# Performance work log

Hardware: AMD Instinct MI355X
Metric: run time of the kernel (lower is better)

The kernel has to match this reference:

```python
import jax, jax.numpy as jnp
import numpy as np

NUM_HEADS = 16


def setup_inputs() -> dict:
    key = jax.random.key(0)
    ks = jax.random.split(key, 5)
    B, S, D = 2, 2048, 1024
    x = jax.random.normal(ks[0], (B, S, D), dtype=jnp.float32)
    # torch Linear weights are [out_features, in_features]; y = x @ W.T + b
    Wq = jax.random.normal(ks[1], (D, D), dtype=jnp.float32) * (D ** -0.5)
    Wk = jax.random.normal(ks[2], (D, D), dtype=jnp.float32) * (D ** -0.5)
    Wv = jax.random.normal(ks[3], (D, D), dtype=jnp.float32) * (D ** -0.5)
    Wo = jax.random.normal(ks[4], (D, D), dtype=jnp.float32) * (D ** -0.5)
    bo = jnp.zeros((D,), dtype=jnp.float32)
    return {"x": x, "Wq": Wq, "Wk": Wk, "Wv": Wv, "Wo": Wo, "bo": bo}


def reference(x, Wq, Wk, Wv, Wo, bo):
    B, S, D = x.shape
    H = NUM_HEADS
    dh = D // H
    # projections (torch Linear: x @ W.T)
    q = (x @ Wq.T).reshape(B, S, H, dh).transpose(0, 2, 1, 3)  # [B,H,S,dh]
    k = (x @ Wk.T).reshape(B, S, H, dh).transpose(0, 2, 1, 3)
    v = (x @ Wv.T).reshape(B, S, H, dh).transpose(0, 2, 1, 3)
    # NOTE: original code takes shape[-1] of the TRANSPOSED key (n,H,dh,S),
    # so the softmax scale is seq_length**-0.5 (a bug we reproduce faithfully).
    scale = jnp.asarray(S, x.dtype) ** -0.5
    scores = jnp.einsum("bhqd,bhkd->bhqk", q, k)  # [B,H,S,S]
    causal = jnp.triu(jnp.ones((S, S), dtype=bool), k=1)
    scores = jnp.where(causal, -jnp.inf, scores * scale)
    weights = jax.nn.softmax(scores, axis=-1)
    # dropout p=0.0 -> identity
    ctx = jnp.einsum("bhqk,bhkd->bhqd", weights, v)  # [B,H,S,dh]
    ctx = ctx.transpose(0, 2, 1, 3).reshape(B, S, D)
    return ctx @ Wo.T + bo
```

## Files before the change

kernel.cpp:

```cpp
#include <hip/hip_runtime.h>
#include <hip/hip_bf16.h>

#define B_SZ    2
#define S_LEN   2048
#define D_MODEL 1024
#define H_NUM   16
#define DH      64
#define M_TOT   (B_SZ * S_LEN)

#define QSCALE (0.022097086912079608f * 1.4426950408889634f)

typedef __attribute__((ext_vector_type(8)))  short          bf16x8;
typedef __attribute__((ext_vector_type(4)))  float          f32x4;
typedef __attribute__((ext_vector_type(16))) float          f32x16;
typedef __attribute__((ext_vector_type(8)))  unsigned short u16x8;
typedef __attribute__((ext_vector_type(4)))  unsigned short u16x4;

__device__ inline unsigned short f2bf(float f) {
  unsigned int u = __float_as_uint(f);
  u += 0x7fffu + ((u >> 16) & 1u);
  return (unsigned short)(u >> 16);
}

__device__ inline float bf2f(unsigned short u) {
  return __uint_as_float(((unsigned)u) << 16);
}

__device__ inline float fexp2(float x) {
#if __has_builtin(__builtin_amdgcn_exp2f)
  return __builtin_amdgcn_exp2f(x);
#else
  return exp2f(x);
#endif
}

__device__ inline unsigned cvt_pk_bf16(float lo, float hi) {
  unsigned r;
  asm("v_cvt_pk_bf16_f32 %0, %1, %2" : "=v"(r) : "v"(lo), "v"(hi));
  return r;
}

__device__ inline void gload16(const void* g, void* l) {
  __builtin_amdgcn_global_load_lds(
      (const __attribute__((address_space(1))) void*)g,
      (__attribute__((address_space(3))) void*)l, 16, 0, 0);
}

__global__ __launch_bounds__(256) void to_bf16_all(
    const float* __restrict__ x, const float* __restrict__ wq,
    const float* __restrict__ wk, const float* __restrict__ wv,
    const float* __restrict__ wo, unsigned short* __restrict__ xb,
    unsigned short* __restrict__ wqb, unsigned short* __restrict__ wkb,
    unsigned short* __restrict__ wvb, unsigned short* __restrict__ wob) {
  const size_t i = ((size_t)blockIdx.x * 256 + threadIdx.x) * 8;
  const float* src;
  unsigned short* dst;
  size_t off;
  if (i < 4194304)      { src = x;  dst = xb;  off = i; }
  else if (i < 5242880) { src = wq; dst = wqb; off = i - 4194304; }
  else if (i < 6291456) { src = wk; dst = wkb; off = i - 5242880; }
  else if (i < 7340032) { src = wv; dst = wvb; off = i - 6291456; }
  else                  { src = wo; dst = wob; off = i - 7340032; }
  f32x4 a = *(const f32x4*)(src + off);
  f32x4 b = *(const f32x4*)(src + off + 4);
  u16x8 o;
#pragma unroll
  for (int j = 0; j < 4; j++) { o[j] = f2bf(a[j]); o[4 + j] = f2bf(b[j]); }
  *(u16x8*)(dst + off) = o;
}

__device__ __forceinline__ void gemm_core(const unsigned short* __restrict__ A,
                                          const unsigned short* __restrict__ W,
                                          unsigned short (*Al)[128][32],
                                          unsigned short (*Bl)[128][32],
                                          int mbase, int nbase,
                                          f32x4 acc[4][4]) {
  const int tid  = threadIdx.x;
  const int lane = tid & 63;
  const int wid  = tid >> 6;
  const int wr   = wid >> 1, wc = wid & 1;
  const int g    = lane >> 4, lr = lane & 15;

  const int r0 = tid >> 2;
  const int cg = (tid & 3) ^ ((tid >> 3) & 3);

  const unsigned short* Abase = A + (size_t)(mbase + r0) * D_MODEL + cg * 8;
  const unsigned short* Wbase = W + (size_t)(nbase + r0) * D_MODEL + cg * 8;
  char* ldsA0 = (char*)Al + wid * 1024;
  char* ldsB0 = (char*)Bl + wid * 1024;

  gload16(Abase, ldsA0);
  gload16(Abase + (size_t)64 * D_MODEL, ldsA0 + 4096);
  gload16(Wbase, ldsB0);
  gload16(Wbase + (size_t)64 * D_MODEL, ldsB0 + 4096);
  gload16(Abase + 32, ldsA0 + 8192);
  gload16(Abase + (size_t)64 * D_MODEL + 32, ldsA0 + 8192 + 4096);
  gload16(Wbase + 32, ldsB0 + 8192);
  gload16(Wbase + (size_t)64 * D_MODEL + 32, ldsB0 + 8192 + 4096);

  const int NKT = D_MODEL / 32;
  int cur = 0, nx2 = 2;
  for (int kt = 0; kt < NKT; ++kt) {
    if (kt + 2 < NKT) {
      const unsigned short* As = Abase + (kt + 2) * 32;
      const unsigned short* Ws = Wbase + (kt + 2) * 32;
      char* la = ldsA0 + nx2 * 8192;
      char* lb = ldsB0 + nx2 * 8192;
      gload16(As, la);
      gload16(As + (size_t)64 * D_MODEL, la + 4096);
      gload16(Ws, lb);
      gload16(Ws + (size_t)64 * D_MODEL, lb + 4096);
      asm volatile("s_waitcnt vmcnt(8)" ::: "memory");
    } else if (kt + 1 < NKT) {
      asm volatile("s_waitcnt vmcnt(4)" ::: "memory");
    } else {
      asm volatile("s_waitcnt vmcnt(0)" ::: "memory");
    }
    __builtin_amdgcn_s_barrier();

    bf16x8 af[4], bfr[4];
#pragma unroll
    for (int i = 0; i < 4; i++) {
      const int ra = wr * 64 + i * 16 + lr;
      af[i] = *(const bf16x8*)&Al[cur][ra][(g ^ ((ra >> 1) & 3)) * 8];
      const int rb = wc * 64 + i * 16 + lr;
      bfr[i] = *(const bf16x8*)&Bl[cur][rb][(g ^ ((rb >> 1) & 3)) * 8];
    }
    __builtin_amdgcn_s_setprio(1);
#pragma unroll
    for (int i = 0; i < 4; i++)
#pragma unroll
      for (int j = 0; j < 4; j++)
        acc[i][j] = __builtin_amdgcn_mfma_f32_16x16x32_bf16(af[i], bfr[j],
                                                            acc[i][j], 0, 0, 0);
    __builtin_amdgcn_s_setprio(0);
    asm volatile("" ::: "memory");
    __builtin_amdgcn_s_barrier();
    cur = (cur == 2) ? 0 : cur + 1;
    nx2 = (nx2 == 2) ? 0 : nx2 + 1;
  }
}

__global__ __launch_bounds__(256) void gemm_qkv(
    const unsigned short* __restrict__ xb, const unsigned short* __restrict__ wqb,
    const unsigned short* __restrict__ wkb, const unsigned short* __restrict__ wvb,
    unsigned short* __restrict__ qb, unsigned short* __restrict__ kb,
    unsigned short* __restrict__ vt) {
  __shared__ unsigned short Al[3][128][32];
  __shared__ unsigned short Bl[3][128][32];
  const int lin = blockIdx.x;
  const int w8  = (lin & 7) * 96 + (lin >> 3);
  const int xq  = w8 & 7;
  const int yq  = (w8 >> 3) & 31;
  const int z   = w8 >> 8;
  const unsigned short* W = (z == 0) ? wqb : (z == 1) ? wkb : wvb;
  unsigned short* dst = (z == 0) ? qb : (z == 1) ? kb : vt;
  const float sc = (z == 0) ? QSCALE : 1.0f;

  f32x4 acc[4][4];
#pragma unroll
  for (int i = 0; i < 4; i++)
#pragma unroll
    for (int j = 0; j < 4; j++) acc[i][j] = (f32x4){0.f, 0.f, 0.f, 0.f};

  const int mbase = yq * 128, nbase = xq * 128;
  gemm_core(xb, W, Al, Bl, mbase, nbase, acc);

  const int lane = threadIdx.x & 63, wid = threadIdx.x >> 6;
  const int wr = wid >> 1, wc = wid & 1, g = lane >> 4, lr = lane & 15;
#pragma unroll
  for (int i = 0; i < 4; i++) {
#pragma unroll
    for (int j = 0; j < 4; j++) {
      const int mg0 = mbase + wr * 64 + i * 16 + g * 4;
      const int ng  = nbase + wc * 64 + j * 16 + lr;
      if (z < 2) {
#pragma unroll
        for (int r = 0; r < 4; r++)
          dst[(size_t)(mg0 + r) * D_MODEL + ng] = f2bf(acc[i][j][r] * sc);
      } else {
        const int hh = ng >> 6, dd = ng & 63;
        const int bb = mg0 >> 11, ss = mg0 & 2047;
        u16x4 pk;
#pragma unroll
        for (int r = 0; r < 4; r++) pk[r] = f2bf(acc[i][j][r]);
        *(u16x4*)&dst[((size_t)((bb * H_NUM + hh) * DH + dd)) * S_LEN + ss] = pk;
      }
    }
  }
}

__global__ __launch_bounds__(256) void gemm_out(
    const unsigned short* __restrict__ cx, const unsigned short* __restrict__ wob,
    float* __restrict__ out, const float* __restrict__ bo) {
  __shared__ unsigned short Al[3][128][32];
  __shared__ unsigned short Bl[3][128][32];
  const int lin = blockIdx.x;
  const int w8  = (lin & 7) * 32 + (lin >> 3);
  const int xq  = w8 & 7;
  const int yq  = w8 >> 3;
  f32x4 acc[4][4];
#pragma unroll
  for (int i = 0; i < 4; i++)
#pragma unroll
    for (int j = 0; j < 4; j++) acc[i][j] = (f32x4){0.f, 0.f, 0.f, 0.f};

  const int mbase = yq * 128, nbase = xq * 128;
  gemm_core(cx, wob, Al, Bl, mbase, nbase, acc);

  const int lane = threadIdx.x & 63, wid = threadIdx.x >> 6;
  const int wr = wid >> 1, wc = wid & 1, g = lane >> 4, lr = lane & 15;
#pragma unroll
  for (int i = 0; i < 4; i++) {
#pragma unroll
    for (int j = 0; j < 4; j++) {
      const int mg0 = mbase + wr * 64 + i * 16 + g * 4;
      const int ng  = nbase + wc * 64 + j * 16 + lr;
      const float bv = bo[ng];
#pragma unroll
      for (int r = 0; r < 4; r++)
        out[(size_t)(mg0 + r) * D_MODEL + ng] = acc[i][j][r] + bv;
    }
  }
}

#define ENT(qi, k0, k1, p) ((unsigned)(qi) | ((unsigned)(k0) << 8) | \
                            ((unsigned)(k1) << 16) | ((unsigned)(p) << 24))
__device__ const unsigned att_sched[40] = {
    ENT(3, 0, 8, 0),   ENT(7, 0, 8, 0),   ENT(7, 8, 16, 1),
    ENT(10, 0, 8, 0),  ENT(11, 0, 8, 0),  ENT(11, 8, 16, 1),
    ENT(11, 16, 24, 2),ENT(14, 0, 8, 0),  ENT(14, 15, 23, 2),
    ENT(15, 0, 8, 0),  ENT(15, 8, 16, 1), ENT(15, 16, 24, 2),
    ENT(15, 24, 32, 3),
    ENT(6, 0, 7, 0),   ENT(6, 7, 14, 1),  ENT(9, 0, 7, 0),
    ENT(9, 7, 14, 1),  ENT(10, 8, 15, 1), ENT(10, 15, 22, 2),
    ENT(12, 0, 7, 0),  ENT(12, 13, 20, 2),ENT(13, 0, 7, 0),
    ENT(13, 7, 14, 1), ENT(13, 14, 21, 2),ENT(13, 21, 28, 3),
    ENT(14, 8, 15, 1), ENT(14, 23, 30, 3),
    ENT(2, 0, 6, 0),   ENT(5, 0, 6, 0),   ENT(5, 6, 12, 1),
    ENT(8, 0, 6, 0),   ENT(8, 6, 12, 1),  ENT(8, 12, 18, 2),
    ENT(9, 14, 20, 2), ENT(12, 7, 13, 1), ENT(12, 20, 26, 3),
    ENT(4, 0, 5, 0),   ENT(4, 5, 10, 1),  ENT(1, 0, 4, 0),
    ENT(0, 0, 2, 0),
};
__device__ const int att_chunks[16]   = {1,1,1,1, 2,2,2,2, 3,3,3,3, 4,4,4,4};
__device__ const int att_mlbase[16]   = {0,1,2,3, 4,6,8,10, 12,15,18,21,
                                         24,28,32,36};
__device__ const int att_opbase[16]   = {0,0,0,0, 0,1,2,3, 4,6,8,10,
                                         12,15,18,21};

__global__ __launch_bounds__(256) void attn_v8(
    const unsigned short* __restrict__ qb, const unsigned short* __restrict__ kb,
    const unsigned short* __restrict__ vt, unsigned short* __restrict__ cx,
    unsigned short* __restrict__ Opart, float* __restrict__ ml) {
  __shared__ alignas(16) char smem[81920];

  const int tid  = threadIdx.x;
  const int lane = tid & 63;
  const int w    = tid >> 6;
  const int hi   = lane >> 5;
  const int lq   = lane & 31;
  const int bid  = blockIdx.x;

  const unsigned ent = att_sched[bid >> 5];
  const int qi   = ent & 255;
  const int kt0  = (ent >> 8) & 255;
  const int kt1  = (ent >> 16) & 255;
  const int part = (ent >> 24) & 255;
  const int nch  = att_chunks[qi];
  const int bh   = bid & 31;
  const int b    = bh >> 4, h = bh & 15;

  const int qg0  = qi * 128 + w * 32;
  const int tok0 = b * S_LEN + qg0;

  const int sr  = tid >> 3;
  const int scg = (tid & 7) ^ (sr & 7);
  const unsigned short* kbase =
      kb + (size_t)(b * S_LEN) * D_MODEL + h * DH + scg * 8;
  const unsigned short* vrow =
      vt + ((size_t)((b * H_NUM + h) * DH + sr)) * S_LEN + scg * 8;
  char* ldsK0 = smem + w * 1024;
  char* ldsV0 = smem + 40960 + w * 1024;

  bf16x8 qf[4];
  {
    const unsigned short* qrow =
        qb + (size_t)(tok0 + lq) * D_MODEL + h * DH + hi * 8;
#pragma unroll
    for (int ks = 0; ks < 4; ks++) qf[ks] = *(const bf16x8*)(qrow + ks * 16);
  }

  f32x16 ctx0, ctx1;
#pragma unroll
  for (int r = 0; r < 16; r++) { ctx0[r] = 0.f; ctx1[r] = 0.f; }
  float l_run = 0.f;

  const int ndiag = 2 * qi;

#pragma unroll
  for (int p = 0; p < 3; p++) {
    if (kt0 + p < kt1) {
      const unsigned short* sK =
          kbase + (size_t)((kt0 + p) * 64 + sr) * D_MODEL;
      gload16(sK, ldsK0 + p * 8192);
      gload16(sK + (size_t)32 * D_MODEL, ldsK0 + p * 8192 + 4096);
      const unsigned short* sV = vrow + (kt0 + p) * 64;
      gload16(sV, ldsV0 + p * 8192);
      gload16(sV + (size_t)32 * S_LEN, ldsV0 + p * 8192 + 4096);
    }
  }

  int cur = 0, nx3 = 3;
  for (int kt = kt0; kt < kt1; ++kt) {
    if (kt + 3 < kt1) {
      const unsigned short* sK = kbase + (size_t)((kt + 3) * 64 + sr) * D_MODEL;
      gload16(sK, ldsK0 + nx3 * 8192);
      gload16(sK + (size_t)32 * D_MODEL, ldsK0 + nx3 * 8192 + 4096);
      const unsigned short* sV = vrow + (kt + 3) * 64;
      gload16(sV, ldsV0 + nx3 * 8192);
      gload16(sV + (size_t)32 * S_LEN, ldsV0 + nx3 * 8192 + 4096);
      asm volatile("s_waitcnt vmcnt(12)" ::: "memory");
    } else if (kt + 2 < kt1) {
      asm volatile("s_waitcnt vmcnt(8)" ::: "memory");
    } else if (kt + 1 < kt1) {
      asm volatile("s_waitcnt vmcnt(4)" ::: "memory");
    } else {
      asm volatile("s_waitcnt vmcnt(0)" ::: "memory");
    }
    __builtin_amdgcn_s_barrier();

    const char* Kc = smem + cur * 8192;
    const char* Vc = smem + 40960 + cur * 8192;

    f32x16 s0, s1;
#pragma unroll
    for (int r = 0; r < 16; r++) { s0[r] = 0.f; s1[r] = 0.f; }
    __builtin_amdgcn_s_setprio(1);
#pragma unroll
    for (int ks = 0; ks < 4; ks++) {
      const int c = ((ks * 2 + hi) ^ (lq & 7)) * 16;
      bf16x8 k0 = *(const bf16x8*)(Kc + lq * 128 + c);
      bf16x8 k1 = *(const bf16x8*)(Kc + (32 + lq) * 128 + c);
      s0 = __builtin_amdgcn_mfma_f32_32x32x16_bf16(k0, qf[ks], s0, 0, 0, 0);
      s1 = __builtin_amdgcn_mfma_f32_32x32x16_bf16(k1, qf[ks], s1, 0, 0, 0);
    }
    __builtin_amdgcn_s_setprio(0);

    if (kt >= ndiag) {
      const int relq = qg0 + lq - kt * 64 - 4 * hi;
#pragma unroll
      for (int r = 0; r < 16; r++) {
        const int ko = (r & 3) + 8 * (r >> 2);
        s0[r] = (ko > relq) ? -1e30f : s0[r];
        s1[r] = (ko + 32 > relq) ? -1e30f : s1[r];
      }
    }

    float lsAcc[4];
#pragma unroll
    for (int ks = 0; ks < 4; ks++) {
      float p[8];
#pragma unroll
      for (int j = 0; j < 8; j++) {
        const int r = (ks & 1) * 8 + j;
        const float sv = (ks < 2) ? s0[r] : s1[r];
        p[j] = fexp2(sv);
      }
      lsAcc[ks] = ((p[0] + p[1]) + (p[2] + p[3])) +
                  ((p[4] + p[5]) + (p[6] + p[7]));
      unsigned a0 = cvt_pk_bf16(p[0], p[1]);
      unsigned a1 = cvt_pk_bf16(p[4], p[5]);
      unsigned b0 = cvt_pk_bf16(p[2], p[3]);
      unsigned b1 = cvt_pk_bf16(p[6], p[7]);
      asm("v_permlane32_swap_b32 %0, %1" : "+v"(a0), "+v"(a1));
      asm("v_permlane32_swap_b32 %0, %1" : "+v"(b0), "+v"(b1));
      union { unsigned u[4]; bf16x8 v; } pw;
      pw.u[0] = a0;
      pw.u[1] = b0;
      pw.u[2] = a1;
      pw.u[3] = b1;
      const int c = ((ks * 2 + hi) ^ (lq & 7)) * 16;
      bf16x8 v0 = *(const bf16x8*)(Vc + lq * 128 + c);
      bf16x8 v1 = *(const bf16x8*)(Vc + (32 + lq) * 128 + c);
      __builtin_amdgcn_s_setprio(1);
      ctx0 = __builtin_amdgcn_mfma_f32_32x32x16_bf16(v0, pw.v, ctx0, 0, 0, 0);
      ctx1 = __builtin_amdgcn_mfma_f32_32x32x16_bf16(v1, pw.v, ctx1, 0, 0, 0);
      __builtin_amdgcn_s_setprio(0);
    }
    l_run += (lsAcc[0] + lsAcc[1]) + (lsAcc[2] + lsAcc[3]);
    cur = (cur == 4) ? 0 : cur + 1;
    nx3 = (nx3 == 4) ? 0 : nx3 + 1;
  }

  __builtin_amdgcn_s_barrier();
  unsigned short (*Tl)[32][72] = (unsigned short (*)[32][72])smem;
  const float lfull = l_run + __shfl_xor(l_run, 32);
  const float inv   = (nch == 1) ? (1.0f / lfull) : 1.0f;
#pragma unroll
  for (int rp = 0; rp < 8; rp++) {
    const int r  = rp * 2;
    const int d0 = (r & 3) + 8 * (r >> 2) + 4 * hi;
    *(unsigned*)&Tl[w][lq][d0] = cvt_pk_bf16(ctx0[r] * inv, ctx0[r + 1] * inv);
    *(unsigned*)&Tl[w][lq][32 + d0] =
        cvt_pk_bf16(ctx1[r] * inv, ctx1[r + 1] * inv);
  }
  asm volatile("s_waitcnt lgkmcnt(0)" ::: "memory");
  const int q2 = lane >> 1;
  unsigned short* dstp;
  if (nch == 1 || part == 0) {
    dstp = &cx[(size_t)(tok0 + q2) * D_MODEL + h * DH];
  } else {
    dstp = Opart + ((size_t)((att_opbase[qi] + part - 1) * 32 + bh) * 128 +
                    w * 32 + q2) * 64;
  }
#pragma unroll
  for (int i = 0; i < 4; i++) {
    const int ch = (lane & 1) * 4 + i;
    u16x8 vv = *(const u16x8*)&Tl[w][q2][ch * 8];
    *(u16x8*)&dstp[ch * 8] = vv;
  }
  if (nch > 1 && hi == 0) {
    float2 v2 = make_float2(0.0f, lfull);
    *(float2*)&ml[((size_t)((att_mlbase[qi] + part) * 32 + bh) * 128 +
                   w * 32 + lq) * 2] = v2;
  }
}

__global__ __launch_bounds__(256) void attn_combine(
    const unsigned short* __restrict__ Opart, const float* __restrict__ ml,
    unsigned short* __restrict__ cx) {
  const int gid = blockIdx.x * 256 + threadIdx.x;
  const int sub = gid & 7;
  const int row = (gid >> 3) & 127;
  const int bh  = (gid >> 10) & 31;
  const int qi  = 4 + (gid >> 15);
  const int nch = att_chunks[qi];
  const int b = bh >> 4, h = bh & 15;
  const int tok = b * S_LEN + qi * 128 + row;

  float denom = 0.f;
#pragma unroll 4
  for (int p = 0; p < 4; p++) {
    if (p < nch) {
      const size_t mi =
          ((size_t)((att_mlbase[qi] + p) * 32 + bh) * 128 + row) * 2;
      denom += ml[mi + 1];
    }
  }
  const float inv = 1.0f / denom;

  float acc[8];
  {
    u16x8 a = *(const u16x8*)&cx[(size_t)tok * D_MODEL + h * DH + sub * 8];
#pragma unroll
    for (int j = 0; j < 8; j++) acc[j] = bf2f(a[j]);
  }
#pragma unroll 4
  for (int p = 1; p < 4; p++) {
    if (p < nch) {
      const unsigned short* src =
          Opart + ((size_t)((att_opbase[qi] + p - 1) * 32 + bh) * 128 + row) * 64;
      u16x8 a = *(const u16x8*)&src[sub * 8];
#pragma unroll
      for (int j = 0; j < 8; j++) acc[j] += bf2f(a[j]);
    }
  }
  u16x8 o;
#pragma unroll
  for (int j = 0; j < 8; j++) o[j] = f2bf(acc[j] * inv);
  *(u16x8*)&cx[(size_t)tok * D_MODEL + h * DH + sub * 8] = o;
}

extern "C" void kernel_launch(void* const* d_in, const int* in_sizes, int n_in,
                              void* d_out, int out_size, void* d_ws,
                              size_t ws_size, hipStream_t stream) {
  const float* x  = (const float*)d_in[0];
  const float* Wq = (const float*)d_in[1];
  const float* Wk = (const float*)d_in[2];
  const float* Wv = (const float*)d_in[3];
  const float* Wo = (const float*)d_in[4];
  const float* bo = (const float*)d_in[5];
  float* out = (float*)d_out;

  unsigned short* xb  = (unsigned short*)d_ws;
  unsigned short* wqb = xb  + (size_t)M_TOT * D_MODEL;
  unsigned short* wkb = wqb + (size_t)D_MODEL * D_MODEL;
  unsigned short* wvb = wkb + (size_t)D_MODEL * D_MODEL;
  unsigned short* wob = wvb + (size_t)D_MODEL * D_MODEL;
  unsigned short* qb  = wob + (size_t)D_MODEL * D_MODEL;
  unsigned short* kb  = qb  + (size_t)M_TOT * D_MODEL;
  unsigned short* vt  = kb  + (size_t)M_TOT * D_MODEL;
  unsigned short* cx  = vt  + (size_t)M_TOT * D_MODEL;
  unsigned short* Opart = xb;
  float*          ml    = (float*)(xb + (size_t)768 * 8192);

  to_bf16_all<<<4096, 256, 0, stream>>>(x, Wq, Wk, Wv, Wo, xb, wqb, wkb, wvb,
                                        wob);
  gemm_qkv<<<dim3(768), 256, 0, stream>>>(xb, wqb, wkb, wvb, qb, kb, vt);
  attn_v8<<<dim3(1280), 256, 0, stream>>>(qb, kb, vt, cx, Opart, ml);
  attn_combine<<<dim3(1536), 256, 0, stream>>>(Opart, ml, cx);
  gemm_out<<<dim3(256), 256, 0, stream>>>(cx, wob, out, bo);
}
```

Before: 110.4 us.

## Use a 4-deep LDS ring in the GEMM core to drop the trailing barrier

The shared GEMM mainloop now uses a 4-slot LDS ring instead of 3 slots, while still prefetching two k-tiles ahead. With the extra slot, the buffer being written is never one another wave may still be reading, so the second barrier at the end of each k-iteration is removed. This halves barrier stalls in the QKV and output projection GEMMs. The cost is LDS per block growing from 48KB to 64KB, which may reduce the number of resident blocks per CU.

```diff
diff --git a/kernel.cpp b/kernel.cpp
--- a/kernel.cpp
+++ b/kernel.cpp
@@ -89,27 +89,24 @@
   char* ldsA0 = (char*)Al + wid * 1024;
   char* ldsB0 = (char*)Bl + wid * 1024;
 
-  gload16(Abase, ldsA0);
-  gload16(Abase + (size_t)64 * D_MODEL, ldsA0 + 4096);
-  gload16(Wbase, ldsB0);
-  gload16(Wbase + (size_t)64 * D_MODEL, ldsB0 + 4096);
-  gload16(Abase + 32, ldsA0 + 8192);
-  gload16(Abase + (size_t)64 * D_MODEL + 32, ldsA0 + 8192 + 4096);
-  gload16(Wbase + 32, ldsB0 + 8192);
-  gload16(Wbase + (size_t)64 * D_MODEL + 32, ldsB0 + 8192 + 4096);
+#define STAGE_G(kt, buf)                                                   \
+  {                                                                        \
+    gload16(Abase + (kt) * 32, ldsA0 + (buf) * 8192);                      \
+    gload16(Abase + (size_t)64 * D_MODEL + (kt) * 32,                      \
+            ldsA0 + (buf) * 8192 + 4096);                                  \
+    gload16(Wbase + (kt) * 32, ldsB0 + (buf) * 8192);                      \
+    gload16(Wbase + (size_t)64 * D_MODEL + (kt) * 32,                      \
+            ldsB0 + (buf) * 8192 + 4096);                                  \
+  }
+
+  STAGE_G(0, 0);
+  STAGE_G(1, 1);
 
   const int NKT = D_MODEL / 32;
   int cur = 0, nx2 = 2;
   for (int kt = 0; kt < NKT; ++kt) {
     if (kt + 2 < NKT) {
-      const unsigned short* As = Abase + (kt + 2) * 32;
-      const unsigned short* Ws = Wbase + (kt + 2) * 32;
-      char* la = ldsA0 + nx2 * 8192;
-      char* lb = ldsB0 + nx2 * 8192;
-      gload16(As, la);
-      gload16(As + (size_t)64 * D_MODEL, la + 4096);
-      gload16(Ws, lb);
-      gload16(Ws + (size_t)64 * D_MODEL, lb + 4096);
+      STAGE_G(kt + 2, nx2);
       asm volatile("s_waitcnt vmcnt(8)" ::: "memory");
     } else if (kt + 1 < NKT) {
       asm volatile("s_waitcnt vmcnt(4)" ::: "memory");
@@ -134,11 +131,10 @@
         acc[i][j] = __builtin_amdgcn_mfma_f32_16x16x32_bf16(af[i], bfr[j],
                                                             acc[i][j], 0, 0, 0);
     __builtin_amdgcn_s_setprio(0);
-    asm volatile("" ::: "memory");
-    __builtin_amdgcn_s_barrier();
-    cur = (cur == 2) ? 0 : cur + 1;
-    nx2 = (nx2 == 2) ? 0 : nx2 + 1;
-  }
+    cur = (cur + 1) & 3;
+    nx2 = (nx2 + 1) & 3;
+  }
+#undef STAGE_G
 }
 
 __global__ __launch_bounds__(256) void gemm_qkv(
@@ -146,8 +142,8 @@
     const unsigned short* __restrict__ wkb, const unsigned short* __restrict__ wvb,
     unsigned short* __restrict__ qb, unsigned short* __restrict__ kb,
     unsigned short* __restrict__ vt) {
-  __shared__ unsigned short Al[3][128][32];
-  __shared__ unsigned short Bl[3][128][32];
+  __shared__ unsigned short Al[4][128][32];
+  __shared__ unsigned short Bl[4][128][32];
   const int lin = blockIdx.x;
   const int w8  = (lin & 7) * 96 + (lin >> 3);
   const int xq  = w8 & 7;
@@ -193,8 +189,8 @@
 __global__ __launch_bounds__(256) void gemm_out(
     const unsigned short* __restrict__ cx, const unsigned short* __restrict__ wob,
     float* __restrict__ out, const float* __restrict__ bo) {
-  __shared__ unsigned short Al[3][128][32];
-  __shared__ unsigned short Bl[3][128][32];
+  __shared__ unsigned short Al[4][128][32];
+  __shared__ unsigned short Bl[4][128][32];
   const int lin = blockIdx.x;
   const int w8  = (lin & 7) * 32 + (lin >> 3);
   const int xq  = w8 & 7;
```

New measurement: 115.6 us. 4.7% more time.
